# Kernel optimization log

Measured on AMD Instinct MI355X. Metric: run time of the kernel, lower is better.

The kernel has to match this reference:

```python
import jax, jax.numpy as jnp
import numpy as np

B, L, S = 4, 512, 100
NG, GS = 19, 5          # 19 clades of 5 species; species 95..99 are singleton clades
VOCAB = 6
HID = 512
HPOOL = 4               # num_attention_heads // 2
D = 64                  # hidden_size / num_attention_heads
ALL = HPOOL * D         # 256
FIRE_H = 32
TIME_SCALE = 1.0        # from time_enc = 'fire_1'
MAX_DIST = 20.0         # config.max_evol_dist


def setup_inputs() -> dict:
    key = jax.random.key(0)
    ks = jax.random.split(key, 10)
    return {
        "source_ids": jax.random.randint(ks[0], (B, L, S), 0, VOCAB, dtype=jnp.int32),
        "in_clade_phylo_dist": jax.random.uniform(ks[1], (S,), dtype=jnp.float32) * MAX_DIST,
        "attn_w_emb": jax.random.normal(ks[2], (VOCAB, HPOOL), dtype=jnp.float32) * 0.02,
        "value_emb": jax.random.normal(ks[3], (VOCAB, ALL), dtype=jnp.float32) * 0.02,
        "ffn_w": jax.random.normal(ks[4], (ALL, HID), dtype=jnp.float32) * 0.02,
        "ffn_b": jnp.zeros((HID,), dtype=jnp.float32),
        "embed_tab": jax.random.normal(ks[5], (VOCAB, HID), dtype=jnp.float32) * 0.02,
        "fire_c": jnp.float32(100.0),
        "fire_w1": jax.random.normal(ks[6], (FIRE_H,), dtype=jnp.float32) * 0.5,
        "fire_w2": jax.random.normal(ks[7], (FIRE_H,), dtype=jnp.float32) * 0.5,
    }


def reference(source_ids, in_clade_phylo_dist, attn_w_emb, value_emb,
              ffn_w, ffn_b, embed_tab, fire_c, fire_w1, fire_w2):
    # --- FIRE time bias: scalar MLP per species distance -> bias[s] ---
    c = jnp.maximum(fire_c, 0.0)
    rel = in_clade_phylo_dist * TIME_SCALE                      # [S]
    rel = jnp.log(c * rel + 1.0) / jnp.log(c * MAX_DIST + 1.0)  # [S]
    h = jax.nn.silu(rel[:, None] * fire_w1[None, :])            # [S, FIRE_H]
    bias = h @ fire_w2                                          # [S]

    # --- multi-species clades: embedding-based attention pooling ---
    grp = jnp.arange(NG * GS).reshape(NG, GS)                   # static clade layout
    ids_g = source_ids[..., :NG * GS].reshape(B, L, NG, GS)     # [B,L,NG,GS]
    scores = jnp.swapaxes(attn_w_emb[ids_g], -1, -2)            # [B,L,NG,H,GS]
    scores = scores + bias[grp][None, None, :, None, :]
    probs = jax.nn.softmax(scores, axis=-1)                     # dropout p=0 (eval)
    vals = value_emb[ids_g].reshape(B, L, NG, GS, HPOOL, D)     # [B,L,NG,GS,H,D]
    pooled = jnp.einsum('blnhg,blnghd->blnhd', probs, vals)     # [B,L,NG,H,D]
    pooled = pooled.reshape(B, L, NG, ALL)
    pooled = pooled @ ffn_w + ffn_b                             # [B,L,NG,HID]

    # --- singleton clades: plain embedding lookup ---
    singles = embed_tab[source_ids[..., NG * GS:]]              # [B,L,5,HID]

    return jnp.concatenate([pooled, singles], axis=-2)          # [B,L,24,HID]
```

## Files before the change

kernel.cpp:

```cpp
#include <hip/hip_runtime.h>

#define B_      4
#define L_      512
#define S_      100
#define NG_     19
#define GS_     5
#define VOCAB_  6
#define HID_    512
#define HPOOL_  4
#define D_      64
#define ALL_    256
#define FIREH_  32
#define MAXDIST_ 20.0f

typedef float f32x2 __attribute__((ext_vector_type(2)));
typedef float f32x4 __attribute__((ext_vector_type(4)));

#define NROWS_  (B_ * L_)

__global__ __launch_bounds__(128) void prep_kernel(
    const float* __restrict__ dist,
    const float* __restrict__ value_emb,
    const float* __restrict__ ffn_w,
    const float* __restrict__ fire_c,
    const float* __restrict__ fire_w1,
    const float* __restrict__ fire_w2,
    float* __restrict__ bias_out,
    float* __restrict__ W2_out)
{
  const int b = blockIdx.x;
  const int t = threadIdx.x;
  if (b < VOCAB_ * HPOOL_ * 4) {
    const int q   = b >> 2;
    const int col = (b & 3) * 128 + t;
    const int v = q >> 2, h = q & 3;
    float acc = 0.f;
#pragma unroll
    for (int k = 0; k < D_; ++k)
      acc = fmaf(value_emb[v * ALL_ + h * D_ + k],
                 ffn_w[(h * D_ + k) * HID_ + col], acc);
    W2_out[q * HID_ + col] = acc;
  } else if (t < S_) {
    const float c = fmaxf(fire_c[0], 0.f);
    const float denom = logf(fmaf(c, MAXDIST_, 1.f));
    const float rel = logf(fmaf(c, dist[t], 1.f)) / denom;
    float acc = 0.f;
#pragma unroll
    for (int i = 0; i < FIREH_; ++i) {
      const float x = rel * fire_w1[i];
      acc = fmaf(x / (1.f + __expf(-x)), fire_w2[i], acc);
    }
    bias_out[t] = acc;
  }
}

#define QB(C, BASE)                                                    \
  a0.x = fmaf(C.x, w2r[BASE + 0].x, a0.x);                             \
  a0.y = fmaf(C.x, w2r[BASE + 0].y, a0.y);                             \
  a1.x = fmaf(C.y, w2r[BASE + 1].x, a1.x);                             \
  a1.y = fmaf(C.y, w2r[BASE + 1].y, a1.y);                             \
  a2.x = fmaf(C.z, w2r[BASE + 2].x, a2.x);                             \
  a2.y = fmaf(C.z, w2r[BASE + 2].y, a2.y);                             \
  a3.x = fmaf(C.w, w2r[BASE + 3].x, a3.x);                             \
  a3.y = fmaf(C.w, w2r[BASE + 3].y, a3.y);

__global__ __launch_bounds__(256, 6) void main_kernel(
    const int*   __restrict__ ids,
    const float* __restrict__ attn_w,
    const float* __restrict__ embed_tab,
    const float* __restrict__ ffn_b,
    const float* __restrict__ bias,
    const float* __restrict__ W2,
    float* __restrict__ out)
{
  const int bl = blockIdx.x;
  const int t  = threadIdx.x;

  __shared__ int   s_ids[S_];
  __shared__ float s_bias[S_];
  __shared__ float s_aw[VOCAB_ * HPOOL_];
  __shared__ __align__(16) float s_cw[NG_][24];

  if (t < S_) s_ids[t] = ids[bl * S_ + t];
  else if (t >= 100 && t < 200) s_bias[t - 100] = bias[t - 100];
  else if (t >= 224 && t < 248) s_aw[t - 224] = attn_w[t - 224];

  f32x2 w2r[24];
#pragma unroll
  for (int q = 0; q < 24; ++q)
    w2r[q] = *(const f32x2*)&W2[q * HID_ + 2 * t];
  const f32x2 bb = *(const f32x2*)&ffn_b[2 * t];

#pragma unroll
  for (int i = t; i < NG_ * 24; i += 256) ((float*)s_cw)[i] = 0.f;
  __syncthreads();

  if (t < NG_ * HPOOL_) {
    const int n = t >> 2, h = t & 3;
    int idg[GS_]; float p[GS_]; float m = -1e30f;
#pragma unroll
    for (int g = 0; g < GS_; ++g) {
      idg[g] = s_ids[n * GS_ + g];
      p[g] = s_aw[idg[g] * HPOOL_ + h] + s_bias[n * GS_ + g];
      m = fmaxf(m, p[g]);
    }
    float s = 0.f;
#pragma unroll
    for (int g = 0; g < GS_; ++g) { p[g] = __expf(p[g] - m); s += p[g]; }
    const float inv = 1.f / s;
#pragma unroll
    for (int g = 0; g < GS_; ++g)
      s_cw[n][idg[g] * HPOOL_ + h] += p[g] * inv;
  }
  __syncthreads();

  float* op = out + (size_t)bl * 24 * HID_ + 2 * t;

#pragma unroll
  for (int j = 0; j < 5; ++j) {
    const int id = s_ids[NG_ * GS_ + j];
    *(f32x2*)(op + (NG_ + j) * HID_) =
        *(const f32x2*)&embed_tab[id * HID_ + 2 * t];
  }

  for (int n = 0; n < NG_; ++n) {
    const f32x4* cw4 = (const f32x4*)s_cw[n];
    const f32x4 c0 = cw4[0], c1 = cw4[1], c2 = cw4[2],
                c3 = cw4[3], c4 = cw4[4], c5 = cw4[5];
    f32x2 a0 = bb;
    f32x2 a1 = {0.f, 0.f}, a2 = {0.f, 0.f}, a3 = {0.f, 0.f};
    QB(c0, 0) QB(c1, 4) QB(c2, 8) QB(c3, 12) QB(c4, 16) QB(c5, 20)
    f32x2 acc;
    acc.x = (a0.x + a1.x) + (a2.x + a3.x);
    acc.y = (a0.y + a1.y) + (a2.y + a3.y);
    *(f32x2*)(op + n * HID_) = acc;
  }
}

extern "C" void kernel_launch(void* const* d_in, const int* in_sizes, int n_in,
                              void* d_out, int out_size, void* d_ws, size_t ws_size,
                              hipStream_t stream) {
  const int*   src_ids = (const int*)  d_in[0];
  const float* dist    = (const float*)d_in[1];
  const float* attn_w  = (const float*)d_in[2];
  const float* valemb  = (const float*)d_in[3];
  const float* ffn_w   = (const float*)d_in[4];
  const float* ffn_b   = (const float*)d_in[5];
  const float* emb_tab = (const float*)d_in[6];
  const float* fire_c  = (const float*)d_in[7];
  const float* fire_w1 = (const float*)d_in[8];
  const float* fire_w2 = (const float*)d_in[9];

  float* out  = (float*)d_out;
  float* ws   = (float*)d_ws;
  float* bias = ws;
  float* W2   = ws + 128;

  hipLaunchKernelGGL(prep_kernel, dim3(97), dim3(128), 0, stream,
                     dist, valemb, ffn_w, fire_c, fire_w1, fire_w2, bias, W2);
  hipLaunchKernelGGL(main_kernel, dim3(NROWS_), dim3(256), 0, stream,
                     src_ids, attn_w, emb_tab, ffn_b, bias, W2, out);
}
```

Before: 32.17 us.

## Process two rows per block with 4-wide column vectors

Each 256-thread block now handles two (b,l) rows, with 128 threads per row each owning four output columns via float4 loads and stores. The grid is halved, so each block's W2 register-load prologue and shared setup cover twice the output and stores are 16 bytes wide. In exchange, each thread holds 24 float4 weight registers and the occupancy hint in launch_bounds is dropped, which raises register pressure and may lower occupancy.

```diff
diff --git a/kernel.cpp b/kernel.cpp
--- a/kernel.cpp
+++ b/kernel.cpp
@@ -54,17 +54,21 @@
   }
 }
 
-#define QB(C, BASE)                                                    \
-  a0.x = fmaf(C.x, w2r[BASE + 0].x, a0.x);                             \
-  a0.y = fmaf(C.x, w2r[BASE + 0].y, a0.y);                             \
-  a1.x = fmaf(C.y, w2r[BASE + 1].x, a1.x);                             \
-  a1.y = fmaf(C.y, w2r[BASE + 1].y, a1.y);                             \
-  a2.x = fmaf(C.z, w2r[BASE + 2].x, a2.x);                             \
-  a2.y = fmaf(C.z, w2r[BASE + 2].y, a2.y);                             \
-  a3.x = fmaf(C.w, w2r[BASE + 3].x, a3.x);                             \
-  a3.y = fmaf(C.w, w2r[BASE + 3].y, a3.y);
+static __device__ __forceinline__ f32x4 fm4(float s, f32x4 w, f32x4 a) {
+  a.x = fmaf(s, w.x, a.x);
+  a.y = fmaf(s, w.y, a.y);
+  a.z = fmaf(s, w.z, a.z);
+  a.w = fmaf(s, w.w, a.w);
+  return a;
+}
 
-__global__ __launch_bounds__(256, 6) void main_kernel(
+#define QB4(C, BASE)                    \
+  a0 = fm4(C.x, w2r[BASE + 0], a0);     \
+  a1 = fm4(C.y, w2r[BASE + 1], a1);     \
+  a2 = fm4(C.z, w2r[BASE + 2], a2);     \
+  a3 = fm4(C.w, w2r[BASE + 3], a3);
+
+__global__ __launch_bounds__(256) void main_kernel(
     const int*   __restrict__ ids,
     const float* __restrict__ attn_w,
     const float* __restrict__ embed_tab,
@@ -73,34 +77,39 @@
     const float* __restrict__ W2,
     float* __restrict__ out)
 {
-  const int bl = blockIdx.x;
-  const int t  = threadIdx.x;
+  const int blk = blockIdx.x;
+  const int t   = threadIdx.x;
+  const int bl0 = blk * 2;
 
-  __shared__ int   s_ids[S_];
+  __shared__ int   s_ids[2 * S_];
   __shared__ float s_bias[S_];
   __shared__ float s_aw[VOCAB_ * HPOOL_];
-  __shared__ __align__(16) float s_cw[NG_][24];
+  __shared__ __align__(16) float s_cw[2][NG_][24];
 
-  if (t < S_) s_ids[t] = ids[bl * S_ + t];
-  else if (t >= 100 && t < 200) s_bias[t - 100] = bias[t - 100];
-  else if (t >= 224 && t < 248) s_aw[t - 224] = attn_w[t - 224];
+  if (t < 2 * S_) s_ids[t] = ids[bl0 * S_ + t];
+  if (t < S_)     s_bias[t] = bias[t];
+  if (t < VOCAB_ * HPOOL_) s_aw[t] = attn_w[t];
 
-  f32x2 w2r[24];
+  const int r  = t >> 7;
+  const int c4 = (t & 127) * 4;
+  f32x4 w2r[24];
 #pragma unroll
   for (int q = 0; q < 24; ++q)
-    w2r[q] = *(const f32x2*)&W2[q * HID_ + 2 * t];
-  const f32x2 bb = *(const f32x2*)&ffn_b[2 * t];
+    w2r[q] = *(const f32x4*)&W2[q * HID_ + c4];
+  const f32x4 bb = *(const f32x4*)&ffn_b[c4];
 
 #pragma unroll
-  for (int i = t; i < NG_ * 24; i += 256) ((float*)s_cw)[i] = 0.f;
+  for (int i = t; i < 2 * NG_ * 24; i += 256) ((float*)s_cw)[i] = 0.f;
   __syncthreads();
 
-  if (t < NG_ * HPOOL_) {
-    const int n = t >> 2, h = t & 3;
+  if (t < 2 * NG_ * HPOOL_) {
+    const int pr = (t >= 76) ? 1 : 0;
+    const int u  = t - 76 * pr;
+    const int n  = u >> 2, h = u & 3;
     int idg[GS_]; float p[GS_]; float m = -1e30f;
 #pragma unroll
     for (int g = 0; g < GS_; ++g) {
-      idg[g] = s_ids[n * GS_ + g];
+      idg[g] = s_ids[pr * S_ + n * GS_ + g];
       p[g] = s_aw[idg[g] * HPOOL_ + h] + s_bias[n * GS_ + g];
       m = fmaxf(m, p[g]);
     }
@@ -110,30 +119,34 @@
     const float inv = 1.f / s;
 #pragma unroll
     for (int g = 0; g < GS_; ++g)
-      s_cw[n][idg[g] * HPOOL_ + h] += p[g] * inv;
+      s_cw[pr][n][idg[g] * HPOOL_ + h] += p[g] * inv;
   }
   __syncthreads();
 
-  float* op = out + (size_t)bl * 24 * HID_ + 2 * t;
+  float* op = out + (size_t)(bl0 + r) * 24 * HID_ + c4;
 
 #pragma unroll
   for (int j = 0; j < 5; ++j) {
-    const int id = s_ids[NG_ * GS_ + j];
-    *(f32x2*)(op + (NG_ + j) * HID_) =
-        *(const f32x2*)&embed_tab[id * HID_ + 2 * t];
+    const int id = s_ids[r * S_ + NG_ * GS_ + j];
+    *(f32x4*)(op + (NG_ + j) * HID_) =
+        *(const f32x4*)&embed_tab[id * HID_ + c4];
   }
 
   for (int n = 0; n < NG_; ++n) {
-    const f32x4* cw4 = (const f32x4*)s_cw[n];
+    const f32x4* cw4 = (const f32x4*)s_cw[r][n];
     const f32x4 c0 = cw4[0], c1 = cw4[1], c2 = cw4[2],
-                c3 = cw4[3], c4 = cw4[4], c5 = cw4[5];
-    f32x2 a0 = bb;
-    f32x2 a1 = {0.f, 0.f}, a2 = {0.f, 0.f}, a3 = {0.f, 0.f};
-    QB(c0, 0) QB(c1, 4) QB(c2, 8) QB(c3, 12) QB(c4, 16) QB(c5, 20)
-    f32x2 acc;
+                c3 = cw4[3], c4v = cw4[4], c5 = cw4[5];
+    f32x4 a0 = bb;
+    f32x4 a1 = {0.f, 0.f, 0.f, 0.f};
+    f32x4 a2 = {0.f, 0.f, 0.f, 0.f};
+    f32x4 a3 = {0.f, 0.f, 0.f, 0.f};
+    QB4(c0, 0) QB4(c1, 4) QB4(c2, 8) QB4(c3, 12) QB4(c4v, 16) QB4(c5, 20)
+    f32x4 acc;
     acc.x = (a0.x + a1.x) + (a2.x + a3.x);
     acc.y = (a0.y + a1.y) + (a2.y + a3.y);
-    *(f32x2*)(op + n * HID_) = acc;
+    acc.z = (a0.z + a1.z) + (a2.z + a3.z);
+    acc.w = (a0.w + a1.w) + (a2.w + a3.w);
+    *(f32x4*)(op + n * HID_) = acc;
   }
 }
 
@@ -158,6 +171,6 @@
 
   hipLaunchKernelGGL(prep_kernel, dim3(97), dim3(128), 0, stream,
                      dist, valemb, ffn_w, fire_c, fire_w1, fire_w2, bias, W2);
-  hipLaunchKernelGGL(main_kernel, dim3(NROWS_), dim3(256), 0, stream,
+  hipLaunchKernelGGL(main_kernel, dim3(NROWS_ / 2), dim3(256), 0, stream,
                      src_ids, attn_w, emb_tab, ffn_b, bias, W2, out);
 }
```

After: 33.36 us. +3.7%, slower.
